# Kernel tuning notes

Measured on AMD Instinct MI355X. Metric: run time of the kernel, lower is better.

Reference implementation:

```python
import jax, jax.numpy as jnp
import numpy as np

B, S, D, H = 4, 2048, 1024, 16
DK = D // H

def setup_inputs() -> dict:
    key = jax.random.key(0)
    ks = jax.random.split(key, 9)
    sc = 1.0 / np.sqrt(D)
    return {
        "X": jax.random.normal(ks[0], (B, S, D), jnp.float32),
        "Wq": jax.random.normal(ks[1], (D, D), jnp.float32) * sc,
        "bq": jax.random.normal(ks[2], (D,), jnp.float32) * 0.01,
        "Wk": jax.random.normal(ks[3], (D, D), jnp.float32) * sc,
        "bk": jax.random.normal(ks[4], (D,), jnp.float32) * 0.01,
        "Wv": jax.random.normal(ks[5], (D, D), jnp.float32) * sc,
        "bv": jax.random.normal(ks[6], (D,), jnp.float32) * 0.01,
        "Wo": jax.random.normal(ks[7], (D, D), jnp.float32) * sc,
        "bo": jax.random.normal(ks[8], (D,), jnp.float32) * 0.01,
    }

def _split_heads(x):
    b, s, d = x.shape
    return x.reshape(b, s, H, DK).transpose(0, 2, 1, 3)  # [B,H,S,DK]

def reference(X, Wq, bq, Wk, bk, Wv, bv, Wo, bo):
    Q = _split_heads(X @ Wq + bq)
    K = _split_heads(X @ Wk + bk)
    V = _split_heads(X @ Wv + bv)
    scores = jnp.einsum('bhqd,bhkd->bhqk', Q, K) / np.sqrt(DK)  # [B,H,S,S]
    probs = jax.nn.softmax(scores, axis=-1)
    Z = jnp.einsum('bhqk,bhkd->bhqd', probs, V)  # [B,H,S,DK]
    Z = Z.transpose(0, 2, 1, 3).reshape(B, S, D)  # combine heads
    return Z @ Wo + bo
```

## Files before the change

kernel.cpp:

```cpp
#include <hip/hip_runtime.h>

#define Bq 4
#define Sq 2048
#define Dq 1024
#define Hq 16
#define Mq (Bq*Sq)

typedef __attribute__((ext_vector_type(2))) _Float16 f16x2;
typedef __attribute__((ext_vector_type(4))) _Float16 f16x4;
typedef __attribute__((ext_vector_type(8))) _Float16 f16x8;
typedef __attribute__((ext_vector_type(4))) float f32x4;

__device__ __forceinline__ f16x2 cvt_pk_f16(float a, float b) {
  return __builtin_bit_cast(f16x2, __builtin_amdgcn_cvt_pkrtz(a, b));
}

__device__ __forceinline__ float fast_exp2(float x) {
#if __has_builtin(__builtin_amdgcn_exp2f)
  return __builtin_amdgcn_exp2f(x);
#else
  float r;
  asm volatile("v_exp_f32 %0, %1" : "=v"(r) : "v"(x));
  return r;
#endif
}

__device__ __forceinline__ void gload16(const _Float16* g, _Float16* l) {
  __builtin_amdgcn_global_load_lds(
      (const __attribute__((address_space(1))) unsigned int*)g,
      (__attribute__((address_space(3))) unsigned int*)l, 16, 0, 0);
}

#define VMCNT(n) asm volatile("s_waitcnt vmcnt(" #n ")" ::: "memory")
#define BARRIER() do { __builtin_amdgcn_s_barrier(); __builtin_amdgcn_sched_barrier(0); } while (0)
#define MFMA32(a, b, c) __builtin_amdgcn_mfma_f32_16x16x32_f16(a, b, c, 0, 0, 0)

__global__ void cvt_f32_f16(const float* __restrict__ in, _Float16* __restrict__ out, int n4) {
  int i = blockIdx.x * blockDim.x + threadIdx.x;
  int stride = gridDim.x * blockDim.x;
  for (; i < n4; i += stride) {
    float4 v = ((const float4*)in)[i];
    f16x4 h = { (_Float16)v.x, (_Float16)v.y, (_Float16)v.z, (_Float16)v.w };
    ((f16x4*)out)[i] = h;
  }
}

__global__ __launch_bounds__(256)
void wt_cvt_all(const float* __restrict__ W0, const float* __restrict__ W1,
                const float* __restrict__ W2, const float* __restrict__ W3,
                _Float16* __restrict__ WTbase) {
  __shared__ _Float16 Tw[64][68];
  const int t = threadIdx.x;
  const int bIdx = (int)blockIdx.x;
  const int w = bIdx >> 8, r = bIdx & 255;
  const int k0 = (r & 15) * 64, n0 = (r >> 4) * 64;
  const float* W = w == 0 ? W0 : (w == 1 ? W1 : (w == 2 ? W2 : W3));
  _Float16* WT = WTbase + (size_t)w * Dq * Dq;
  #pragma unroll
  for (int i = 0; i < 4; i++) {
    int row = (t >> 4) + 16 * i;
    float4 v = *(const float4*)(W + (size_t)(k0 + row) * Dq + n0 + (t & 15) * 4);
    f16x4 h = { (_Float16)v.x, (_Float16)v.y, (_Float16)v.z, (_Float16)v.w };
    *(f16x4*)&Tw[row][(t & 15) * 4] = h;
  }
  __syncthreads();
  const int n = t & 63, ks = t >> 6;
  f16x8 v0, v1;
  #pragma unroll
  for (int j = 0; j < 8; j++) { v0[j] = Tw[ks * 16 + j][n]; v1[j] = Tw[ks * 16 + 8 + j][n]; }
  _Float16* dst = WT + (size_t)(n0 + n) * Dq + k0 + ks * 16;
  *(f16x8*)dst = v0;
  *(f16x8*)(dst + 8) = v1;
}

__global__ __launch_bounds__(256, 3)
void qkv_gemm(const _Float16* __restrict__ A, const _Float16* __restrict__ WTall,
              const float* __restrict__ bq, const float* __restrict__ bk,
              const float* __restrict__ bv, _Float16* __restrict__ Qh,
              _Float16* __restrict__ Kh, _Float16* __restrict__ Vth, float qscale) {
  __shared__ alignas(16) char smem[33280];
  _Float16* As = (_Float16*)smem;
  _Float16* Bs = (_Float16*)(smem + 16384);
  const int tid = threadIdx.x, wid = tid >> 6, lane = tid & 63;
  const int wr = wid >> 1, wc = wid & 1;
  const int lq = lane & 15, g = lane >> 4;
  int bid = (int)blockIdx.x;
  bid = (bid & 7) * 192 + (bid >> 3);
  const int bx = bid % 24, by = bid / 24;
  const int row0 = by * 128, col0 = bx * 128;

  const int srow = lane >> 3;
  const int schunk = (lane & 7) ^ srow;
  const _Float16* Ag = A     + (size_t)(row0 + 32 * wid + srow) * Dq + schunk * 8;
  const _Float16* Bg = WTall + (size_t)(col0 + 32 * wid + srow) * Dq + schunk * 8;
  _Float16* AsW = As + (32 * wid) * 64;
  _Float16* BsW = Bs + (32 * wid) * 64;

  f32x4 acc[4][4];
  #pragma unroll
  for (int m = 0; m < 4; m++)
    #pragma unroll
    for (int n = 0; n < 4; n++) acc[m][n] = (f32x4){0.f, 0.f, 0.f, 0.f};

  for (int k0 = 0; k0 < Dq; k0 += 64) {
    __syncthreads();
    #pragma unroll
    for (int i = 0; i < 4; i++) {
      gload16(Ag + k0 + (size_t)(8 * i) * Dq, AsW + (8 * i) * 64);
      gload16(Bg + k0 + (size_t)(8 * i) * Dq, BsW + (8 * i) * 64);
    }
    __syncthreads();
    #pragma unroll
    for (int s = 0; s < 2; s++) {
      f16x8 a[4], b[4];
      #pragma unroll
      for (int m = 0; m < 4; m++) {
        int row = wr * 64 + m * 16 + lq;
        a[m] = *(const f16x8*)&As[row * 64 + (((4 * s + g) ^ (lq & 7)) * 8)];
      }
      #pragma unroll
      for (int n = 0; n < 4; n++) {
        int row = wc * 64 + n * 16 + lq;
        b[n] = *(const f16x8*)&Bs[row * 64 + (((4 * s + g) ^ (lq & 7)) * 8)];
      }
      #pragma unroll
      for (int m = 0; m < 4; m++)
        #pragma unroll
        for (int n = 0; n < 4; n++)
          acc[m][n] = MFMA32(a[m], b[n], acc[m][n]);
    }
  }

  const int rid = col0 >> 10, lcol0 = col0 & 1023;
  const float* bp = rid == 0 ? bq : (rid == 1 ? bk : bv);
  const float scl = rid == 0 ? qscale : 1.0f;

  if (rid < 2) {
    _Float16* Cc = rid == 0 ? Qh : Kh;
    #pragma unroll
    for (int m = 0; m < 4; m++)
      #pragma unroll
      for (int n = 0; n < 4; n++) {
        int col = lcol0 + wc * 64 + n * 16 + lq;
        float bvv = bp[col];
        #pragma unroll
        for (int r = 0; r < 4; r++) {
          int row = row0 + wr * 64 + m * 16 + 4 * g + r;
          Cc[(size_t)row * Dq + col] = (_Float16)((acc[m][n][r] + bvv) * scl);
        }
      }
  } else {
    _Float16* Ts = (_Float16*)smem;
    __syncthreads();
    #pragma unroll
    for (int m = 0; m < 4; m++)
      #pragma unroll
      for (int n = 0; n < 4; n++) {
        int c = wc * 64 + n * 16 + lq;
        float bvv = bp[lcol0 + c];
        #pragma unroll
        for (int r = 0; r < 4; r++) {
          int s = wr * 64 + m * 16 + 4 * g + r;
          Ts[s * 130 + c] = (_Float16)(acc[m][n][r] + bvv);
        }
      }
    __syncthreads();
    const int b = row0 >> 11, stile = (row0 & 2047) >> 7;
    #pragma unroll
    for (int i = 0; i < 8; i++) {
      int idx = i * 256 + tid;
      int hh = idx >> 10, c = idx & 1023;
      int kk = c >> 8, nd = (c >> 6) & 3, gg = (c >> 4) & 3, lqq = c & 15;
      int d = nd * 16 + lqq;
      f16x8 v;
      #pragma unroll
      for (int j = 0; j < 8; j++) {
        int sl = 32 * kk + 16 * (j >> 2) + 4 * gg + (j & 3);
        v[j] = Ts[sl * 130 + hh * 64 + d];
      }
      int hHead = (lcol0 >> 6) + hh;
      size_t off = (((size_t)(b * Hq + hHead) * 16 + stile) * 1024 + c) * 8;
      *(f16x8*)(Vth + off) = v;
    }
  }
}

__global__ __launch_bounds__(256, 3)
void out_gemm(const _Float16* __restrict__ A, const _Float16* __restrict__ WT,
              const float* __restrict__ bias, float* __restrict__ Cf) {
  __shared__ alignas(16) char smem[32768];
  _Float16* As = (_Float16*)smem;
  _Float16* Bs = (_Float16*)(smem + 16384);
  const int tid = threadIdx.x, wid = tid >> 6, lane = tid & 63;
  const int wr = wid >> 1, wc = wid & 1;
  const int lq = lane & 15, g = lane >> 4;
  int bid = (int)blockIdx.x;
  bid = (bid & 7) * 64 + (bid >> 3);
  const int bx = bid & 7, by = bid >> 3;
  const int row0 = by * 128, col0 = bx * 128;

  const int srow = lane >> 3;
  const int schunk = (lane & 7) ^ srow;
  const _Float16* Ag = A  + (size_t)(row0 + 32 * wid + srow) * Dq + schunk * 8;
  const _Float16* Bg = WT + (size_t)(col0 + 32 * wid + srow) * Dq + schunk * 8;
  _Float16* AsW = As + (32 * wid) * 64;
  _Float16* BsW = Bs + (32 * wid) * 64;

  f32x4 acc[4][4];
  #pragma unroll
  for (int m = 0; m < 4; m++)
    #pragma unroll
    for (int n = 0; n < 4; n++) acc[m][n] = (f32x4){0.f, 0.f, 0.f, 0.f};

  for (int k0 = 0; k0 < Dq; k0 += 64) {
    __syncthreads();
    #pragma unroll
    for (int i = 0; i < 4; i++) {
      gload16(Ag + k0 + (size_t)(8 * i) * Dq, AsW + (8 * i) * 64);
      gload16(Bg + k0 + (size_t)(8 * i) * Dq, BsW + (8 * i) * 64);
    }
    __syncthreads();
    #pragma unroll
    for (int s = 0; s < 2; s++) {
      f16x8 a[4], b[4];
      #pragma unroll
      for (int m = 0; m < 4; m++) {
        int row = wr * 64 + m * 16 + lq;
        a[m] = *(const f16x8*)&As[row * 64 + (((4 * s + g) ^ (lq & 7)) * 8)];
      }
      #pragma unroll
      for (int n = 0; n < 4; n++) {
        int row = wc * 64 + n * 16 + lq;
        b[n] = *(const f16x8*)&Bs[row * 64 + (((4 * s + g) ^ (lq & 7)) * 8)];
      }
      #pragma unroll
      for (int m = 0; m < 4; m++)
        #pragma unroll
        for (int n = 0; n < 4; n++)
          acc[m][n] = MFMA32(a[m], b[n], acc[m][n]);
    }
  }

  #pragma unroll
  for (int m = 0; m < 4; m++)
    #pragma unroll
    for (int n = 0; n < 4; n++) {
      int col = col0 + wc * 64 + n * 16 + lq;
      float bvv = bias[col];
      #pragma unroll
      for (int r = 0; r < 4; r++) {
        int row = row0 + wr * 64 + m * 16 + 4 * g + r;
        Cf[(size_t)row * Dq + col] = acc[m][n][r] + bvv;
      }
    }
}

__global__ __launch_bounds__(256, 4)
void attn_kernel(const _Float16* __restrict__ Q, const _Float16* __restrict__ K,
                 const _Float16* __restrict__ Vt, _Float16* __restrict__ Z) {
  __shared__ alignas(16) char smem[32768];
  _Float16* const sm = (_Float16*)smem;
  const int tid = threadIdx.x, wid = tid >> 6, lane = tid & 63;
  const int lq = lane & 15, g = lane >> 4;
  const int id = (int)blockIdx.x;
  const int qb = (id >> 3) & 15;
  const int hb = (id & 7) + 8 * (id >> 7);
  const int h = hb & 15, b = hb >> 4;
  const int q0 = qb * 128;
  const int bh = b * Hq + h;

  const _Float16* Qr0 = Q + (size_t)(b * Sq + q0 + wid * 32 + lq) * Dq + h * 64;
  const _Float16* Qr1 = Qr0 + (size_t)16 * Dq;
  const f16x8 Qf00 = *(const f16x8*)(Qr0 + 8 * g);
  const f16x8 Qf01 = *(const f16x8*)(Qr0 + 32 + 8 * g);
  const f16x8 Qf10 = *(const f16x8*)(Qr1 + 8 * g);
  const f16x8 Qf11 = *(const f16x8*)(Qr1 + 32 + 8 * g);
  VMCNT(0);

  const int krow = tid >> 3;
  const int kch = (tid & 7) ^ (krow & 7);
  const _Float16* Kg = K + (size_t)(b * Sq + krow) * Dq + h * 64 + kch * 8;
  const _Float16* Vg = Vt + (size_t)bh * 16 * 8192;

  const int e7 = lq & 7;
  const int cq0 = (g ^ e7) * 8, cq1 = ((4 + g) ^ e7) * 8;

  f32x4 zacc[2][4];
  #pragma unroll
  for (int gq = 0; gq < 2; gq++)
    #pragma unroll
    for (int nd = 0; nd < 4; nd++) zacc[gq][nd] = (f32x4){0.f, 0.f, 0.f, 0.f};
  f32x4 lsum0 = (f32x4){0.f, 0.f, 0.f, 0.f};
  f32x4 lsum1 = (f32x4){0.f, 0.f, 0.f, 0.f};
  const f32x4 fz = (f32x4){0.f, 0.f, 0.f, 0.f};
  f16x8 ones;
  #pragma unroll
  for (int j = 0; j < 8; j++) ones[j] = (_Float16)1.0f;

  auto stageK = [&](int t, int buf) {
    _Float16* Kd = sm + buf * 4096;
    const _Float16* ks = Kg + (size_t)t * 64 * Dq;
    gload16(ks, Kd + tid * 8);
    gload16(ks + (size_t)32 * Dq, Kd + 2048 + tid * 8);
  };
  auto stageV = [&](int t, int buf) {
    _Float16* Vd = sm + 8192 + buf * 4096;
    const _Float16* vs = Vg + (size_t)(t >> 1) * 8192 + (t & 1) * 4096 + tid * 8;
    gload16(vs, Vd + tid * 8);
    gload16(vs + 2048, Vd + 2048 + tid * 8);
  };

  stageK(0, 0);
  stageV(0, 0);
  stageK(1, 1);
  stageV(1, 1);

  #pragma unroll 2
  for (int t = 0; t < 32; ++t) {
    const int buf = t & 1;
    const _Float16* Kb = sm + buf * 4096;
    const _Float16* Vb = sm + 8192 + buf * 4096;

    if (t < 31) { VMCNT(4); } else { VMCNT(0); }
    BARRIER();

    f32x4 sacc[2][4];
    __builtin_amdgcn_s_setprio(1);
    #pragma unroll
    for (int rb = 0; rb < 4; ++rb) {
      const _Float16* rbp = Kb + (rb * 16 + lq) * 64;
      f16x8 a0 = *(const f16x8*)(rbp + cq0);
      f16x8 a1 = *(const f16x8*)(rbp + cq1);
      sacc[0][rb] = MFMA32(a0, Qf00, fz);
      sacc[0][rb] = MFMA32(a1, Qf01, sacc[0][rb]);
      sacc[1][rb] = MFMA32(a0, Qf10, fz);
      sacc[1][rb] = MFMA32(a1, Qf11, sacc[1][rb]);
    }
    __builtin_amdgcn_s_setprio(0);

    f16x8 pb[2][2];
    #pragma unroll
    for (int gq = 0; gq < 2; ++gq)
      #pragma unroll
      for (int kkL = 0; kkL < 2; ++kkL) {
        const f32x4 sa = sacc[gq][kkL * 2], sb = sacc[gq][kkL * 2 + 1];
        f16x2 c0 = cvt_pk_f16(fast_exp2(sa[0]), fast_exp2(sa[1]));
        f16x2 c1 = cvt_pk_f16(fast_exp2(sa[2]), fast_exp2(sa[3]));
        f16x2 c2 = cvt_pk_f16(fast_exp2(sb[0]), fast_exp2(sb[1]));
        f16x2 c3 = cvt_pk_f16(fast_exp2(sb[2]), fast_exp2(sb[3]));
        f16x8 p8;
        p8[0] = c0[0]; p8[1] = c0[1]; p8[2] = c1[0]; p8[3] = c1[1];
        p8[4] = c2[0]; p8[5] = c2[1]; p8[6] = c3[0]; p8[7] = c3[1];
        pb[gq][kkL] = p8;
      }

    __builtin_amdgcn_s_setprio(1);
    #pragma unroll
    for (int kkL = 0; kkL < 2; ++kkL) {
      lsum0 = MFMA32(ones, pb[0][kkL], lsum0);
      lsum1 = MFMA32(ones, pb[1][kkL], lsum1);
      #pragma unroll
      for (int nd = 0; nd < 4; ++nd) {
        f16x8 av = *(const f16x8*)(Vb + kkL * 2048 + nd * 512 + lane * 8);
        zacc[0][nd] = MFMA32(av, pb[0][kkL], zacc[0][nd]);
        zacc[1][nd] = MFMA32(av, pb[1][kkL], zacc[1][nd]);
      }
    }
    __builtin_amdgcn_s_setprio(0);

    BARRIER();
    if (t < 30) { stageK(t + 2, buf); stageV(t + 2, buf); }
  }

  const float inv0 = 1.0f / lsum0[0];
  const float inv1 = 1.0f / lsum1[0];
  __syncthreads();
  _Float16* Zs = sm;
  #pragma unroll
  for (int gq = 0; gq < 2; gq++) {
    const float inv = gq == 0 ? inv0 : inv1;
    #pragma unroll
    for (int nd = 0; nd < 4; nd++) {
      f16x4 zv;
      #pragma unroll
      for (int r = 0; r < 4; r++) zv[r] = (_Float16)(zacc[gq][nd][r] * inv);
      *(f16x4*)&Zs[(wid * 32 + gq * 16 + lq) * 72 + nd * 16 + 4 * g] = zv;
    }
  }
  __syncthreads();
  const int row = tid >> 1, half = tid & 1;
  const _Float16* zr = &Zs[row * 72 + half * 32];
  f16x8 v0 = *(const f16x8*)zr;
  f16x8 v1 = *(const f16x8*)(zr + 8);
  f16x8 v2 = *(const f16x8*)(zr + 16);
  f16x8 v3 = *(const f16x8*)(zr + 24);
  _Float16* dst = Z + (size_t)(b * Sq + q0 + row) * Dq + h * 64 + half * 32;
  *(f16x8*)dst = v0;
  *(f16x8*)(dst + 8) = v1;
  *(f16x8*)(dst + 16) = v2;
  *(f16x8*)(dst + 24) = v3;
}

extern "C" void kernel_launch(void* const* d_in, const int* in_sizes, int n_in,
                              void* d_out, int out_size, void* d_ws, size_t ws_size,
                              hipStream_t stream) {
  const float* X  = (const float*)d_in[0];
  const float* Wq = (const float*)d_in[1];
  const float* bq = (const float*)d_in[2];
  const float* Wk = (const float*)d_in[3];
  const float* bk = (const float*)d_in[4];
  const float* Wv = (const float*)d_in[5];
  const float* bv = (const float*)d_in[6];
  const float* Wo = (const float*)d_in[7];
  const float* bo = (const float*)d_in[8];

  _Float16* Xh   = (_Float16*)d_ws;
  _Float16* WqT  = Xh   + (size_t)Mq * Dq;
  _Float16* WoT  = WqT  + (size_t)3 * Dq * Dq;
  _Float16* Qh   = WoT  + (size_t)Dq * Dq;
  _Float16* Kh   = Qh   + (size_t)Mq * Dq;
  _Float16* Vth  = Kh   + (size_t)Mq * Dq;
  _Float16* Zh   = Vth  + (size_t)Mq * Dq;

  cvt_f32_f16<<<dim3(2048), dim3(256), 0, stream>>>(X, Xh, (int)((size_t)Mq * Dq / 4));
  wt_cvt_all<<<dim3(1024), dim3(256), 0, stream>>>(Wq, Wk, Wv, Wo, WqT);

  const float qscale = 0.125f * 1.44269504088896f;
  qkv_gemm<<<dim3(1536), dim3(256), 0, stream>>>(Xh, WqT, bq, bk, bv, Qh, Kh, Vth, qscale);

  attn_kernel<<<dim3(1024), dim3(256), 0, stream>>>(Qh, Kh, Vth, Zh);

  out_gemm<<<dim3(512), dim3(256), 0, stream>>>(Zh, WoT, bo, (float*)d_out);
}
```

Baseline: 168.4 us.

## Use two waves of 64 query rows per attention block to reuse K/V fragments

The attention kernel now runs 128 threads per block, with each wave handling 64 query rows (four 16-row groups) instead of 32. Each K and V fragment read from LDS feeds twice as many MFMAs. Global staging loads per thread double to cover the same 64-key tiles, and the wait count is adjusted to match. This raises register pressure and halves the waves per block, which may reduce occupancy and latency hiding.

```diff
diff --git a/kernel.cpp b/kernel.cpp
--- a/kernel.cpp
+++ b/kernel.cpp
@@ -255,7 +255,7 @@
     }
 }
 
-__global__ __launch_bounds__(256, 4)
+__global__ __launch_bounds__(128, 2)
 void attn_kernel(const _Float16* __restrict__ Q, const _Float16* __restrict__ K,
                  const _Float16* __restrict__ Vt, _Float16* __restrict__ Z) {
   __shared__ alignas(16) char smem[32768];
@@ -269,12 +269,13 @@
   const int q0 = qb * 128;
   const int bh = b * Hq + h;
 
-  const _Float16* Qr0 = Q + (size_t)(b * Sq + q0 + wid * 32 + lq) * Dq + h * 64;
-  const _Float16* Qr1 = Qr0 + (size_t)16 * Dq;
-  const f16x8 Qf00 = *(const f16x8*)(Qr0 + 8 * g);
-  const f16x8 Qf01 = *(const f16x8*)(Qr0 + 32 + 8 * g);
-  const f16x8 Qf10 = *(const f16x8*)(Qr1 + 8 * g);
-  const f16x8 Qf11 = *(const f16x8*)(Qr1 + 32 + 8 * g);
+  f16x8 Qf[4][2];
+  #pragma unroll
+  for (int g4 = 0; g4 < 4; ++g4) {
+    const _Float16* Qr = Q + (size_t)(b * Sq + q0 + wid * 64 + g4 * 16 + lq) * Dq + h * 64;
+    Qf[g4][0] = *(const f16x8*)(Qr + 8 * g);
+    Qf[g4][1] = *(const f16x8*)(Qr + 32 + 8 * g);
+  }
   VMCNT(0);
 
   const int krow = tid >> 3;
@@ -285,13 +286,14 @@
   const int e7 = lq & 7;
   const int cq0 = (g ^ e7) * 8, cq1 = ((4 + g) ^ e7) * 8;
 
-  f32x4 zacc[2][4];
-  #pragma unroll
-  for (int gq = 0; gq < 2; gq++)
-    #pragma unroll
-    for (int nd = 0; nd < 4; nd++) zacc[gq][nd] = (f32x4){0.f, 0.f, 0.f, 0.f};
-  f32x4 lsum0 = (f32x4){0.f, 0.f, 0.f, 0.f};
-  f32x4 lsum1 = (f32x4){0.f, 0.f, 0.f, 0.f};
+  f32x4 zacc[4][4];
+  #pragma unroll
+  for (int g4 = 0; g4 < 4; g4++)
+    #pragma unroll
+    for (int nd = 0; nd < 4; nd++) zacc[g4][nd] = (f32x4){0.f, 0.f, 0.f, 0.f};
+  f32x4 lsum[4];
+  #pragma unroll
+  for (int g4 = 0; g4 < 4; g4++) lsum[g4] = (f32x4){0.f, 0.f, 0.f, 0.f};
   const f32x4 fz = (f32x4){0.f, 0.f, 0.f, 0.f};
   f16x8 ones;
   #pragma unroll
@@ -300,14 +302,16 @@
   auto stageK = [&](int t, int buf) {
     _Float16* Kd = sm + buf * 4096;
     const _Float16* ks = Kg + (size_t)t * 64 * Dq;
-    gload16(ks, Kd + tid * 8);
-    gload16(ks + (size_t)32 * Dq, Kd + 2048 + tid * 8);
+    #pragma unroll
+    for (int i = 0; i < 4; ++i)
+      gload16(ks + (size_t)(16 * i) * Dq, Kd + i * 1024 + tid * 8);
   };
   auto stageV = [&](int t, int buf) {
     _Float16* Vd = sm + 8192 + buf * 4096;
     const _Float16* vs = Vg + (size_t)(t >> 1) * 8192 + (t & 1) * 4096 + tid * 8;
-    gload16(vs, Vd + tid * 8);
-    gload16(vs + 2048, Vd + 2048 + tid * 8);
+    #pragma unroll
+    for (int i = 0; i < 4; ++i)
+      gload16(vs + i * 1024, Vd + i * 1024 + tid * 8);
   };
 
   stageK(0, 0);
@@ -321,29 +325,30 @@
     const _Float16* Kb = sm + buf * 4096;
     const _Float16* Vb = sm + 8192 + buf * 4096;
 
-    if (t < 31) { VMCNT(4); } else { VMCNT(0); }
+    if (t < 31) { VMCNT(8); } else { VMCNT(0); }
     BARRIER();
 
-    f32x4 sacc[2][4];
+    f32x4 sacc[4][4];
     __builtin_amdgcn_s_setprio(1);
     #pragma unroll
     for (int rb = 0; rb < 4; ++rb) {
       const _Float16* rbp = Kb + (rb * 16 + lq) * 64;
       f16x8 a0 = *(const f16x8*)(rbp + cq0);
       f16x8 a1 = *(const f16x8*)(rbp + cq1);
-      sacc[0][rb] = MFMA32(a0, Qf00, fz);
-      sacc[0][rb] = MFMA32(a1, Qf01, sacc[0][rb]);
-      sacc[1][rb] = MFMA32(a0, Qf10, fz);
-      sacc[1][rb] = MFMA32(a1, Qf11, sacc[1][rb]);
+      #pragma unroll
+      for (int g4 = 0; g4 < 4; ++g4) {
+        sacc[g4][rb] = MFMA32(a0, Qf[g4][0], fz);
+        sacc[g4][rb] = MFMA32(a1, Qf[g4][1], sacc[g4][rb]);
+      }
     }
     __builtin_amdgcn_s_setprio(0);
 
-    f16x8 pb[2][2];
-    #pragma unroll
-    for (int gq = 0; gq < 2; ++gq)
+    f16x8 pb[4][2];
+    #pragma unroll
+    for (int g4 = 0; g4 < 4; ++g4)
       #pragma unroll
       for (int kkL = 0; kkL < 2; ++kkL) {
-        const f32x4 sa = sacc[gq][kkL * 2], sb = sacc[gq][kkL * 2 + 1];
+        const f32x4 sa = sacc[g4][kkL * 2], sb = sacc[g4][kkL * 2 + 1];
         f16x2 c0 = cvt_pk_f16(fast_exp2(sa[0]), fast_exp2(sa[1]));
         f16x2 c1 = cvt_pk_f16(fast_exp2(sa[2]), fast_exp2(sa[3]));
         f16x2 c2 = cvt_pk_f16(fast_exp2(sb[0]), fast_exp2(sb[1]));
@@ -351,19 +356,21 @@
         f16x8 p8;
         p8[0] = c0[0]; p8[1] = c0[1]; p8[2] = c1[0]; p8[3] = c1[1];
         p8[4] = c2[0]; p8[5] = c2[1]; p8[6] = c3[0]; p8[7] = c3[1];
-        pb[gq][kkL] = p8;
+        pb[g4][kkL] = p8;
       }
 
     __builtin_amdgcn_s_setprio(1);
     #pragma unroll
     for (int kkL = 0; kkL < 2; ++kkL) {
-      lsum0 = MFMA32(ones, pb[0][kkL], lsum0);
-      lsum1 = MFMA32(ones, pb[1][kkL], lsum1);
+      #pragma unroll
+      for (int g4 = 0; g4 < 4; ++g4)
+        lsum[g4] = MFMA32(ones, pb[g4][kkL], lsum[g4]);
       #pragma unroll
       for (int nd = 0; nd < 4; ++nd) {
         f16x8 av = *(const f16x8*)(Vb + kkL * 2048 + nd * 512 + lane * 8);
-        zacc[0][nd] = MFMA32(av, pb[0][kkL], zacc[0][nd]);
-        zacc[1][nd] = MFMA32(av, pb[1][kkL], zacc[1][nd]);
+        #pragma unroll
+        for (int g4 = 0; g4 < 4; ++g4)
+          zacc[g4][nd] = MFMA32(av, pb[g4][kkL], zacc[g4][nd]);
       }
     }
     __builtin_amdgcn_s_setprio(0);
@@ -372,33 +379,26 @@
     if (t < 30) { stageK(t + 2, buf); stageV(t + 2, buf); }
   }
 
-  const float inv0 = 1.0f / lsum0[0];
-  const float inv1 = 1.0f / lsum1[0];
   __syncthreads();
   _Float16* Zs = sm;
   #pragma unroll
-  for (int gq = 0; gq < 2; gq++) {
-    const float inv = gq == 0 ? inv0 : inv1;
+  for (int g4 = 0; g4 < 4; g4++) {
+    const float inv = 1.0f / lsum[g4][0];
     #pragma unroll
     for (int nd = 0; nd < 4; nd++) {
       f16x4 zv;
       #pragma unroll
-      for (int r = 0; r < 4; r++) zv[r] = (_Float16)(zacc[gq][nd][r] * inv);
-      *(f16x4*)&Zs[(wid * 32 + gq * 16 + lq) * 72 + nd * 16 + 4 * g] = zv;
+      for (int r = 0; r < 4; r++) zv[r] = (_Float16)(zacc[g4][nd][r] * inv);
+      *(f16x4*)&Zs[(wid * 64 + g4 * 16 + lq) * 72 + nd * 16 + 4 * g] = zv;
     }
   }
   __syncthreads();
-  const int row = tid >> 1, half = tid & 1;
-  const _Float16* zr = &Zs[row * 72 + half * 32];
-  f16x8 v0 = *(const f16x8*)zr;
-  f16x8 v1 = *(const f16x8*)(zr + 8);
-  f16x8 v2 = *(const f16x8*)(zr + 16);
-  f16x8 v3 = *(const f16x8*)(zr + 24);
-  _Float16* dst = Z + (size_t)(b * Sq + q0 + row) * Dq + h * 64 + half * 32;
-  *(f16x8*)dst = v0;
-  *(f16x8*)(dst + 8) = v1;
-  *(f16x8*)(dst + 16) = v2;
-  *(f16x8*)(dst + 24) = v3;
+  const int row = tid;
+  const _Float16* zr = &Zs[row * 72];
+  _Float16* dst = Z + (size_t)(b * Sq + q0 + row) * Dq + h * 64;
+  #pragma unroll
+  for (int j = 0; j < 8; ++j)
+    *(f16x8*)(dst + j * 8) = *(const f16x8*)(zr + j * 8);
 }
 
 extern "C" void kernel_launch(void* const* d_in, const int* in_sizes, int n_in,
@@ -428,7 +428,7 @@
   const float qscale = 0.125f * 1.44269504088896f;
   qkv_gemm<<<dim3(1536), dim3(256), 0, stream>>>(Xh, WqT, bq, bk, bv, Qh, Kh, Vth, qscale);
 
-  attn_kernel<<<dim3(1024), dim3(256), 0, stream>>>(Qh, Kh, Vth, Zh);
+  attn_kernel<<<dim3(1024), dim3(128), 0, stream>>>(Qh, Kh, Vth, Zh);
 
   out_gemm<<<dim3(512), dim3(256), 0, stream>>>(Zh, WoT, bo, (float*)d_out);
 }
```

Measured after the change: 171.4 us. Within noise of the previous version (+1.8%).

## Software-pipeline attention PV stage with triple-buffered V and merge prep kernels

Applied to the files above, without the earlier changes.

The attention loop is restructured so that the P·V MFMAs for the previous tile run right after the QK^T MFMAs of the current tile. This overlaps the exp/convert softmax work with matrix-core work, and the P·V step for the final tile moves to an epilogue after the loop. V staging goes from double to triple buffering, which raises LDS from 32 KB to 40 KB and could lower occupancy. Separately, the X conversion and the weight transpose/convert kernels are merged into one launch to remove a kernel launch and let the two run together.

```diff
diff --git a/kernel.cpp b/kernel.cpp
--- a/kernel.cpp
+++ b/kernel.cpp
@@ -35,42 +35,44 @@
 #define BARRIER() do { __builtin_amdgcn_s_barrier(); __builtin_amdgcn_sched_barrier(0); } while (0)
 #define MFMA32(a, b, c) __builtin_amdgcn_mfma_f32_16x16x32_f16(a, b, c, 0, 0, 0)
 
-__global__ void cvt_f32_f16(const float* __restrict__ in, _Float16* __restrict__ out, int n4) {
-  int i = blockIdx.x * blockDim.x + threadIdx.x;
-  int stride = gridDim.x * blockDim.x;
-  for (; i < n4; i += stride) {
-    float4 v = ((const float4*)in)[i];
-    f16x4 h = { (_Float16)v.x, (_Float16)v.y, (_Float16)v.z, (_Float16)v.w };
-    ((f16x4*)out)[i] = h;
-  }
-}
-
 __global__ __launch_bounds__(256)
-void wt_cvt_all(const float* __restrict__ W0, const float* __restrict__ W1,
-                const float* __restrict__ W2, const float* __restrict__ W3,
-                _Float16* __restrict__ WTbase) {
+void prep_all(const float* __restrict__ X, const float* __restrict__ W0,
+              const float* __restrict__ W1, const float* __restrict__ W2,
+              const float* __restrict__ W3, _Float16* __restrict__ Xh,
+              _Float16* __restrict__ WTbase) {
   __shared__ _Float16 Tw[64][68];
   const int t = threadIdx.x;
   const int bIdx = (int)blockIdx.x;
-  const int w = bIdx >> 8, r = bIdx & 255;
-  const int k0 = (r & 15) * 64, n0 = (r >> 4) * 64;
-  const float* W = w == 0 ? W0 : (w == 1 ? W1 : (w == 2 ? W2 : W3));
-  _Float16* WT = WTbase + (size_t)w * Dq * Dq;
-  #pragma unroll
-  for (int i = 0; i < 4; i++) {
-    int row = (t >> 4) + 16 * i;
-    float4 v = *(const float4*)(W + (size_t)(k0 + row) * Dq + n0 + (t & 15) * 4);
-    f16x4 h = { (_Float16)v.x, (_Float16)v.y, (_Float16)v.z, (_Float16)v.w };
-    *(f16x4*)&Tw[row][(t & 15) * 4] = h;
-  }
-  __syncthreads();
-  const int n = t & 63, ks = t >> 6;
-  f16x8 v0, v1;
-  #pragma unroll
-  for (int j = 0; j < 8; j++) { v0[j] = Tw[ks * 16 + j][n]; v1[j] = Tw[ks * 16 + 8 + j][n]; }
-  _Float16* dst = WT + (size_t)(n0 + n) * Dq + k0 + ks * 16;
-  *(f16x8*)dst = v0;
-  *(f16x8*)(dst + 8) = v1;
+  if (bIdx < 1024) {
+    const int w = bIdx >> 8, r = bIdx & 255;
+    const int k0 = (r & 15) * 64, n0 = (r >> 4) * 64;
+    const float* W = w == 0 ? W0 : (w == 1 ? W1 : (w == 2 ? W2 : W3));
+    _Float16* WT = WTbase + (size_t)w * Dq * Dq;
+    #pragma unroll
+    for (int i = 0; i < 4; i++) {
+      int row = (t >> 4) + 16 * i;
+      float4 v = *(const float4*)(W + (size_t)(k0 + row) * Dq + n0 + (t & 15) * 4);
+      f16x4 h = { (_Float16)v.x, (_Float16)v.y, (_Float16)v.z, (_Float16)v.w };
+      *(f16x4*)&Tw[row][(t & 15) * 4] = h;
+    }
+    __syncthreads();
+    const int n = t & 63, ks = t >> 6;
+    f16x8 v0, v1;
+    #pragma unroll
+    for (int j = 0; j < 8; j++) { v0[j] = Tw[ks * 16 + j][n]; v1[j] = Tw[ks * 16 + 8 + j][n]; }
+    _Float16* dst = WT + (size_t)(n0 + n) * Dq + k0 + ks * 16;
+    *(f16x8*)dst = v0;
+    *(f16x8*)(dst + 8) = v1;
+  } else {
+    const int n4 = (int)((size_t)Mq * Dq / 4);
+    int i = (bIdx - 1024) * 256 + t;
+    const int stride = 2048 * 256;
+    for (; i < n4; i += stride) {
+      float4 v = ((const float4*)X)[i];
+      f16x4 h = { (_Float16)v.x, (_Float16)v.y, (_Float16)v.z, (_Float16)v.w };
+      ((f16x4*)Xh)[i] = h;
+    }
+  }
 }
 
 __global__ __launch_bounds__(256, 3)
@@ -258,7 +260,7 @@
 __global__ __launch_bounds__(256, 4)
 void attn_kernel(const _Float16* __restrict__ Q, const _Float16* __restrict__ K,
                  const _Float16* __restrict__ Vt, _Float16* __restrict__ Z) {
-  __shared__ alignas(16) char smem[32768];
+  __shared__ alignas(16) char smem[40960];
   _Float16* const sm = (_Float16*)smem;
   const int tid = threadIdx.x, wid = tid >> 6, lane = tid & 63;
   const int lq = lane & 15, g = lane >> 4;
@@ -303,8 +305,8 @@
     gload16(ks, Kd + tid * 8);
     gload16(ks + (size_t)32 * Dq, Kd + 2048 + tid * 8);
   };
-  auto stageV = [&](int t, int buf) {
-    _Float16* Vd = sm + 8192 + buf * 4096;
+  auto stageV = [&](int t, int vb) {
+    _Float16* Vd = sm + 8192 + vb * 4096;
     const _Float16* vs = Vg + (size_t)(t >> 1) * 8192 + (t & 1) * 4096 + tid * 8;
     gload16(vs, Vd + tid * 8);
     gload16(vs + 2048, Vd + 2048 + tid * 8);
@@ -315,11 +317,18 @@
   stageK(1, 1);
   stageV(1, 1);
 
+  f16x8 pbp[2][2];
+  #pragma unroll
+  for (int gq = 0; gq < 2; gq++)
+    #pragma unroll
+    for (int kkL = 0; kkL < 2; kkL++) pbp[gq][kkL] = ones;
+  int vuse = 0;
+  int vst = 2;
+
   #pragma unroll 2
   for (int t = 0; t < 32; ++t) {
-    const int buf = t & 1;
-    const _Float16* Kb = sm + buf * 4096;
-    const _Float16* Vb = sm + 8192 + buf * 4096;
+    const int kb = t & 1;
+    const _Float16* Kb = sm + kb * 4096;
 
     if (t < 31) { VMCNT(4); } else { VMCNT(0); }
     BARRIER();
@@ -336,9 +345,24 @@
       sacc[1][rb] = MFMA32(a0, Qf10, fz);
       sacc[1][rb] = MFMA32(a1, Qf11, sacc[1][rb]);
     }
+
+    if (t > 0) {
+      const _Float16* Vb = sm + 8192 + vuse * 4096;
+      #pragma unroll
+      for (int kkL = 0; kkL < 2; ++kkL) {
+        lsum0 = MFMA32(ones, pbp[0][kkL], lsum0);
+        lsum1 = MFMA32(ones, pbp[1][kkL], lsum1);
+        #pragma unroll
+        for (int nd = 0; nd < 4; ++nd) {
+          f16x8 av = *(const f16x8*)(Vb + kkL * 2048 + nd * 512 + lane * 8);
+          zacc[0][nd] = MFMA32(av, pbp[0][kkL], zacc[0][nd]);
+          zacc[1][nd] = MFMA32(av, pbp[1][kkL], zacc[1][nd]);
+        }
+      }
+      vuse = vuse == 2 ? 0 : vuse + 1;
+    }
     __builtin_amdgcn_s_setprio(0);
 
-    f16x8 pb[2][2];
     #pragma unroll
     for (int gq = 0; gq < 2; ++gq)
       #pragma unroll
@@ -351,25 +375,32 @@
         f16x8 p8;
         p8[0] = c0[0]; p8[1] = c0[1]; p8[2] = c1[0]; p8[3] = c1[1];
         p8[4] = c2[0]; p8[5] = c2[1]; p8[6] = c3[0]; p8[7] = c3[1];
-        pb[gq][kkL] = p8;
-      }
-
+        pbp[gq][kkL] = p8;
+      }
+
+    BARRIER();
+    if (t < 30) {
+      stageK(t + 2, kb);
+      stageV(t + 2, vst);
+      vst = vst == 2 ? 0 : vst + 1;
+    }
+  }
+
+  {
+    const _Float16* Vb = sm + 8192 + vuse * 4096;
     __builtin_amdgcn_s_setprio(1);
     #pragma unroll
     for (int kkL = 0; kkL < 2; ++kkL) {
-      lsum0 = MFMA32(ones, pb[0][kkL], lsum0);
-      lsum1 = MFMA32(ones, pb[1][kkL], lsum1);
+      lsum0 = MFMA32(ones, pbp[0][kkL], lsum0);
+      lsum1 = MFMA32(ones, pbp[1][kkL], lsum1);
       #pragma unroll
       for (int nd = 0; nd < 4; ++nd) {
         f16x8 av = *(const f16x8*)(Vb + kkL * 2048 + nd * 512 + lane * 8);
-        zacc[0][nd] = MFMA32(av, pb[0][kkL], zacc[0][nd]);
-        zacc[1][nd] = MFMA32(av, pb[1][kkL], zacc[1][nd]);
+        zacc[0][nd] = MFMA32(av, pbp[0][kkL], zacc[0][nd]);
+        zacc[1][nd] = MFMA32(av, pbp[1][kkL], zacc[1][nd]);
       }
     }
     __builtin_amdgcn_s_setprio(0);
-
-    BARRIER();
-    if (t < 30) { stageK(t + 2, buf); stageV(t + 2, buf); }
   }
 
   const float inv0 = 1.0f / lsum0[0];
@@ -422,8 +453,7 @@
   _Float16* Vth  = Kh   + (size_t)Mq * Dq;
   _Float16* Zh   = Vth  + (size_t)Mq * Dq;
 
-  cvt_f32_f16<<<dim3(2048), dim3(256), 0, stream>>>(X, Xh, (int)((size_t)Mq * Dq / 4));
-  wt_cvt_all<<<dim3(1024), dim3(256), 0, stream>>>(Wq, Wk, Wv, Wo, WqT);
+  prep_all<<<dim3(3072), dim3(256), 0, stream>>>(X, Wq, Wk, Wv, Wo, Xh, WqT);
 
   const float qscale = 0.125f * 1.44269504088896f;
   qkv_gemm<<<dim3(1536), dim3(256), 0, stream>>>(Xh, WqT, bq, bk, bv, Qh, Kh, Vth, qscale);
```

Result: no change. 169.9 us (+0.9%).
